# Kernel tuning notes

Hardware: AMD Instinct MI355X
Metric: run time of the kernel (lower is better)

Reference implementation:

```python
import jax, jax.numpy as jnp
from jax import lax
import numpy as np

T, B, IN, H = 192, 16, 256, 256


def setup_inputs() -> dict:
    key = jax.random.key(0)
    ks = jax.random.split(key, 8)
    s = 0.05  # small init scale to keep gates well-conditioned
    return {
        "x": jax.random.normal(ks[0], (T, B, IN), dtype=jnp.float32),
        # shared LSTM (PyTorch gate order i,f,g,o)
        "W_ih": jax.random.normal(ks[1], (4 * H, IN), dtype=jnp.float32) * s,
        "W_hh": jax.random.normal(ks[2], (4 * H, H), dtype=jnp.float32) * s,
        "b_lstm": jnp.zeros((4 * H,), dtype=jnp.float32),
        # additive attention: Ws: (IN+2H)->H, Us: H->1
        "Ws_w": jax.random.normal(ks[3], (H, IN + 2 * H), dtype=jnp.float32) * s,
        "Ws_b": jnp.zeros((H,), dtype=jnp.float32),
        "Us_w": jax.random.normal(ks[4], (1, H), dtype=jnp.float32) * s,
        "Us_b": jnp.zeros((1,), dtype=jnp.float32),
        # task-specific message LSTM cell: gates from concat(x_t, Rt, h_prev)
        "Wc": jax.random.normal(ks[5], (4 * H, IN + 2 * H), dtype=jnp.float32) * s,
        "bc": jnp.zeros((4 * H,), dtype=jnp.float32),
        "TASK": 0,
    }


def _lstm_gates(pre, c):
    i, f, g, o = jnp.split(pre, 4, axis=-1)
    i = jax.nn.sigmoid(i)
    f = jax.nn.sigmoid(f)
    g = jnp.tanh(g)
    o = jax.nn.sigmoid(o)
    c_new = f * c + i * g
    h_new = o * jnp.tanh(c_new)
    return h_new, c_new


def reference(x, W_ih, W_hh, b_lstm, Ws_w, Ws_b, Us_w, Us_b, Wc, bc, TASK):
    t_len, b, _ = x.shape
    h = W_hh.shape[1]

    h0 = jnp.zeros((b, h), x.dtype)

    # ---- shared LSTM over time ----
    def shared_step(carry, xt):
        hh, cc = carry
        pre = xt @ W_ih.T + hh @ W_hh.T + b_lstm
        hh, cc = _lstm_gates(pre, cc)
        return (hh, cc), hh

    (_, _), hs = lax.scan(shared_step, (h0, h0), x)  # hs: [T,B,H]

    # ---- per-timestep additive attention + message LSTM cell ----
    def task_step(carry, xt):
        hh, cc = carry
        h_task = jnp.broadcast_to(hh[None], (t_len, b, h))
        cat = jnp.concatenate([hs, h_task, x], axis=-1)          # [T,B,IN+2H]
        score = jnp.tanh(cat @ Ws_w.T + Ws_b) @ Us_w.T + Us_b    # [T,B,1]
        att = jax.nn.softmax(score, axis=0)                       # over time
        Rt = jnp.sum(att * hs, axis=0)                            # [B,H]
        pre = jnp.concatenate([xt, Rt, hh], axis=-1) @ Wc.T + bc
        hh, cc = _lstm_gates(pre, cc)
        return (hh, cc), hh

    (_, _), outs = lax.scan(task_step, (h0, h0), x)  # [T,B,H]
    return jnp.transpose(outs, (1, 0, 2))  # [B,T,H] (torch.stack axis=1)
```

## Files before the change

kernel.cpp:

```cpp
#include <hip/hip_runtime.h>
#include <hip/hip_fp16.h>

#define T_LEN 192

typedef unsigned long long u64;
typedef _Float16 f16x8 __attribute__((ext_vector_type(8)));
typedef float f32x4 __attribute__((ext_vector_type(4)));

#define OFF_X1F   0
#define OFF_XPRE  3145728
#define OFF_XB3   6291456
#define OFF_HSB   7077888
#define OFF_P     7864320
#define OFF_H     7921664
#define OFF_HX    7929856
#define OFF_HP    7946240
#define EXCH_WORDS 147456

#define SMEM_TASK 148736

__device__ __forceinline__ unsigned packh2(float a, float b){
  union { __half2 h; unsigned u; } v;
  v.h = __halves2half2(__float2half(a), __float2half(b));
  return v.u;
}
__device__ __forceinline__ float2 unp2(unsigned u){
  union { unsigned u32; __half2 h; } v; v.u32 = u;
  return __half22float2(v.h);
}
__device__ __forceinline__ float fdot2(unsigned a, unsigned b, float c){
#if __has_builtin(__builtin_amdgcn_fdot2)
  typedef _Float16 h2t __attribute__((ext_vector_type(2)));
  union { unsigned u; h2t h; } ua, ub;
  ua.u = a; ub.u = b;
  return __builtin_amdgcn_fdot2(ua.h, ub.h, c, false);
#else
  float2 x = unp2(a), y = unp2(b);
  return c + x.x*y.x + x.y*y.y;
#endif
}
__device__ __forceinline__ float tanh_f(float x){
  float cx = fminf(fmaxf(x, -15.f), 15.f);
  float e = __expf(2.f * cx);
  return (e - 1.f) / (e + 1.f);
}
__device__ __forceinline__ float sigm(float x){
  float cx = fminf(fmaxf(x, -30.f), 30.f);
  return 1.f / (1.f + __expf(-cx));
}

__device__ __forceinline__ u64 gld64(const u64* p){
  return __hip_atomic_load(p, __ATOMIC_RELAXED, __HIP_MEMORY_SCOPE_AGENT);
}
__device__ __forceinline__ void gst64(u64* p, u64 v){
  __hip_atomic_store(p, v, __ATOMIC_RELAXED, __HIP_MEMORY_SCOPE_AGENT);
}

__global__ __launch_bounds__(256) void initk(float* p, int n){
  int i = blockIdx.x * blockDim.x + threadIdx.x;
  int stride = gridDim.x * blockDim.x;
  for (; i < n; i += stride) p[i] = 0.f;
}

__global__ __launch_bounds__(256) void proj3m(const float* __restrict__ x,
                                              const float* __restrict__ W_ih,
                                              const float* __restrict__ b_l,
                                              const float* __restrict__ Wc,
                                              const float* __restrict__ bc,
                                              const float* __restrict__ Ws_w,
                                              const float* __restrict__ Ws_b,
                                              float* __restrict__ ws){
  __shared__ unsigned xhi[16 * 136];
  __shared__ unsigned xlo[16 * 136];
  const int bx = blockIdx.x, t = blockIdx.y, tid = threadIdx.x;

  {
    int row = tid >> 4, c0 = (tid & 15) * 16;
    const float* xp = &x[(t * 16 + row) * 256 + c0];
    #pragma unroll
    for (int i = 0; i < 8; ++i) {
      float2 v = *(const float2*)&xp[2 * i];
      _Float16 h0 = (_Float16)v.x, h1 = (_Float16)v.y;
      float l0 = v.x - (float)h0, l1 = v.y - (float)h1;
      union { _Float16 h[2]; unsigned u; } ph, pl;
      ph.h[0] = h0; ph.h[1] = h1;
      pl.h[0] = (_Float16)l0; pl.h[1] = (_Float16)l1;
      xhi[row * 136 + c0 / 2 + i] = ph.u;
      xlo[row * 136 + c0 / 2 + i] = pl.u;
    }
  }

  const int wave = tid >> 6, lane = tid & 63;
  const int b16 = lane & 15, quad = lane >> 4;
  const int n0 = bx * 64 + wave * 16;
  const float* wrow; const float* bias; int nb, mode;
  if (bx < 16)      { nb = n0;        wrow = &W_ih[(nb + b16) * 256];       bias = b_l;  mode = 0; }
  else if (bx < 32) { nb = n0 - 1024; wrow = &Wc[(nb + b16) * 768];         bias = bc;   mode = 1; }
  else              { nb = n0 - 2048; wrow = &Ws_w[(nb + b16) * 768 + 512]; bias = Ws_b; mode = 2; }

  f16x8 whi[8], wlo[8];
  #pragma unroll
  for (int kk = 0; kk < 8; ++kk) {
    const float* wp = wrow + kk * 32 + quad * 8;
    f16x8 h, l;
    #pragma unroll
    for (int j = 0; j < 8; ++j) {
      float v = wp[j];
      _Float16 hh = (_Float16)v;
      h[j] = hh; l[j] = (_Float16)(v - (float)hh);
    }
    whi[kk] = h; wlo[kk] = l;
  }
  f32x4 acc;
  #pragma unroll
  for (int r = 0; r < 4; ++r) acc[r] = bias[nb + quad * 4 + r];
  __syncthreads();

  #pragma unroll
  for (int kk = 0; kk < 8; ++kk) {
    union { uint4 u; f16x8 h; } bh, bl;
    bh.u = *(const uint4*)&xhi[b16 * 136 + kk * 16 + quad * 4];
    bl.u = *(const uint4*)&xlo[b16 * 136 + kk * 16 + quad * 4];
    acc = __builtin_amdgcn_mfma_f32_16x16x32_f16(whi[kk], bh.h, acc, 0, 0, 0);
    acc = __builtin_amdgcn_mfma_f32_16x16x32_f16(wlo[kk], bh.h, acc, 0, 0, 0);
    acc = __builtin_amdgcn_mfma_f32_16x16x32_f16(whi[kk], bl.h, acc, 0, 0, 0);
  }

  float4 res; res.x = acc[0]; res.y = acc[1]; res.z = acc[2]; res.w = acc[3];
  if (mode == 0) {
    *(float4*)&ws[OFF_X1F + (((u64)t * 64 + (n0 >> 4)) * 16 + b16) * 16 + quad * 4] = res;
  } else if (mode == 1) {
    *(float4*)&ws[OFF_XPRE + ((u64)t * 16 + b16) * 1024 + nb + quad * 4] = res;
  } else {
    *(float4*)&ws[OFF_XB3 + ((u64)t * 16 + b16) * 256 + nb + quad * 4] = res;
  }
}

__global__ __launch_bounds__(512) void lstm_kernel(const float* __restrict__ X1F,
                                                   const float* __restrict__ W_hh,
                                                   float* __restrict__ hsB,
                                                   u64* __restrict__ hx){
  __shared__ unsigned hT[16 * 136];
  const int tid = threadIdx.x;
  const int wg = blockIdx.x;
  const int wave = tid >> 6, lane = tid & 63;
  const int b16 = lane & 15, quad = lane >> 4;
  const int jb = wg * 8 + wave;
  const int peerbase = (1 - wg) * 64;

  f16x8 wf[4][8];
  #pragma unroll
  for (int g = 0; g < 4; ++g) {
    #pragma unroll
    for (int kk = 0; kk < 8; ++kk) {
      int row = g * 256 + jb * 16 + b16;
      const float* wp = &W_hh[row * 256 + kk * 32 + quad * 8];
      f16x8 v;
      #pragma unroll
      for (int j = 0; j < 8; ++j) v[j] = (_Float16)wp[j];
      wf[g][kk] = v;
    }
  }
  for (int i = tid; i < 16 * 136; i += 512) hT[i] = 0u;
  float cst[4] = {0.f, 0.f, 0.f, 0.f};
  __syncthreads();

  for (int t = 0; t < T_LEN; ++t) {
    float4 xi[4];
    #pragma unroll
    for (int g = 0; g < 4; ++g)
      xi[g] = *(const float4*)&X1F[((t * 64 + g * 16 + jb) * 16 + b16) * 16 + quad * 4];

    if (t > 0) {
      const u64* src = &hx[((u64)((t - 1) & 1)) * 2048];
      int bbq = tid >> 5, k2 = tid & 31;
      int jp0 = peerbase + 2 * k2;
      u64 v0, v1;
      for (;;) {
        v0 = gld64(&src[bbq * 128 + jp0]);
        v1 = gld64(&src[bbq * 128 + jp0 + 1]);
        if ((unsigned)v0 == (unsigned)t && (unsigned)v1 == (unsigned)t) break;
      }
      hT[bbq * 136 + jp0]     = (unsigned)(v0 >> 32);
      hT[bbq * 136 + jp0 + 1] = (unsigned)(v1 >> 32);
    }
    __syncthreads();

    f32x4 acc[4];
    #pragma unroll
    for (int g = 0; g < 4; ++g) {
      f32x4 a; a[0]=xi[g].x; a[1]=xi[g].y; a[2]=xi[g].z; a[3]=xi[g].w;
      acc[g] = a;
    }
    #pragma unroll
    for (int kk = 0; kk < 8; ++kk) {
      union { uint4 u; f16x8 h; } bv;
      bv.u = *(const uint4*)&hT[b16 * 136 + kk * 16 + quad * 4];
      #pragma unroll
      for (int g = 0; g < 4; ++g)
        acc[g] = __builtin_amdgcn_mfma_f32_16x16x32_f16(wf[g][kk], bv.h, acc[g], 0, 0, 0);
    }
    __syncthreads();

    float hv[4];
    #pragma unroll
    for (int r = 0; r < 4; ++r) {
      float pi = acc[0][r], pf = acc[1][r], pg = acc[2][r], po = acc[3][r];
      float cn = fmaf(sigm(pf), cst[r], sigm(pi) * tanh_f(pg));
      hv[r] = sigm(po) * tanh_f(cn);
      cst[r] = cn;
    }
    int j0 = jb * 16 + quad * 4;
    int jp = j0 >> 1;
    unsigned p01 = packh2(hv[0], hv[1]);
    unsigned p23 = packh2(hv[2], hv[3]);
    u64* dst = &hx[((u64)(t & 1)) * 2048];
    gst64(&dst[b16 * 128 + jp],     ((u64)p01 << 32) | (unsigned)(t + 1));
    gst64(&dst[b16 * 128 + jp + 1], ((u64)p23 << 32) | (unsigned)(t + 1));
    *(float4*)&hsB[(b16 * 192 + t) * 256 + j0] = make_float4(hv[0], hv[1], hv[2], hv[3]);
    hT[b16 * 136 + jp]     = p01;
    hT[b16 * 136 + jp + 1] = p23;
  }
}

__global__ __launch_bounds__(1024) void task_kernel(
    const float* __restrict__ xb3, const float* __restrict__ xpre,
    const float* __restrict__ hsB, const float* __restrict__ Us_w,
    const float* __restrict__ Us_b, const float* __restrict__ Wc,
    const float* __restrict__ Ws_w,
    u64* __restrict__ Pbuf, u64* __restrict__ Hbuf, u64* __restrict__ HPbuf,
    float* __restrict__ out){
  extern __shared__ char smem[];
  unsigned* hsL  = (unsigned*)smem;
  unsigned* Ws1L = (unsigned*)(smem + 99072);
  float*    baseS= (float*)(smem + 115584);
  unsigned* WcH  = (unsigned*)smem;
  unsigned* Ws2P = (unsigned*)(smem + 65536);
  float* prel    = (float*)(smem + 82944);
  float* eel     = (float*)(smem + 89600);
  unsigned* h2l  = (unsigned*)(smem + 90368);
  unsigned* h2own= (unsigned*)(smem + 90880);
  float* hterml  = (float*)(smem + 90944);
  float* usl     = (float*)(smem + 91072);
  float* msc     = (float*)(smem + 91200);
  unsigned* G2   = (unsigned*)(smem + 99072);

  const int tid = threadIdx.x;
  const int bb = blockIdx.x & 15;
  const int s  = blockIdx.x >> 4;

  for (int idx = tid; idx < 24576; idx += 1024) {
    int tp = idx >> 7, k2 = idx & 127;
    const float* hp = &hsB[(bb * 192 + tp) * 256 + 2 * k2];
    hsL[tp * 129 + k2] = packh2(hp[0], hp[1]);
  }
  for (int idx = tid; idx < 4096; idx += 1024) {
    int c = idx >> 7, k2 = idx & 127;
    const float* wp = &Ws_w[(32 * s + c) * 768 + 2 * k2];
    Ws1L[c * 129 + k2] = packh2(wp[0], wp[1]);
  }
  __syncthreads();
  {
    int c = tid & 31, g = tid >> 5;
    float a6[6];
    #pragma unroll
    for (int j = 0; j < 6; ++j)
      a6[j] = xb3[((g * 6 + j) * 16 + bb) * 256 + 32 * s + c];
    for (int k2 = 0; k2 < 128; ++k2) {
      unsigned wv = Ws1L[c * 129 + k2];
      #pragma unroll
      for (int j = 0; j < 6; ++j)
        a6[j] = fdot2(wv, hsL[(g * 6 + j) * 129 + k2], a6[j]);
    }
    #pragma unroll
    for (int j = 0; j < 6; ++j)
      baseS[(g * 6 + j) * 33 + c] = a6[j];
  }
  __syncthreads();
  unsigned bs4[4] = {0u, 0u, 0u, 0u};
  if (tid < 768) {
    int tp = tid >> 2, q = tid & 3;
    #pragma unroll
    for (int j2 = 0; j2 < 4; ++j2)
      bs4[j2] = packh2(baseS[tp * 33 + q * 8 + 2 * j2],
                       baseS[tp * 33 + q * 8 + 2 * j2 + 1]);
  }
  __syncthreads();
  {
    int l = tid & 127, tg = tid >> 7;
    int row = (l >> 5) * 256 + 32 * s + (l & 31);
    const float* wr = &Wc[row * 768 + 256];
    float acc[24];
    #pragma unroll
    for (int i = 0; i < 24; ++i) acc[i] = 0.f;
    for (int kc = 0; kc < 128; kc += 16) {
      unsigned wv[16];
      #pragma unroll
      for (int i = 0; i < 16; ++i) {
        float2 wp2 = *(const float2*)&wr[2 * (kc + i)];
        wv[i] = packh2(wp2.x, wp2.y);
      }
      #pragma unroll
      for (int tt = 0; tt < 24; ++tt) {
        const unsigned* hp = &hsL[(tg * 24 + tt) * 129 + kc];
        float a = acc[tt];
        #pragma unroll
        for (int i = 0; i < 16; ++i) a = fdot2(wv[i], hp[i], a);
        acc[tt] = a;
      }
    }
    #pragma unroll
    for (int i = 0; i < 12; ++i)
      G2[l * 97 + tg * 12 + i] = packh2(acc[2 * i], acc[2 * i + 1]);
  }
  __syncthreads();
  for (int idx = tid; idx < 16384; idx += 1024) {
    int j = idx & 3, l = (idx >> 2) & 127, k2q = idx >> 9;
    int k2 = k2q * 4 + j;
    int row = (l >> 5) * 256 + 32 * s + (l & 31);
    const float* wp = &Wc[row * 768 + 512 + 2 * k2];
    WcH[idx] = packh2(wp[0], wp[1]);
  }
  for (int idx = tid; idx < 4096; idx += 1024) {
    int c = idx >> 4, j = idx & 15;
    const float* wp = &Ws_w[c * 768 + 256 + 2 * (16 * s + j)];
    Ws2P[c * 17 + j] = packh2(wp[0], wp[1]);
  }
  if (tid < 32) usl[tid] = Us_w[32 * s + tid];
  const float usb = Us_b[0];
  __syncthreads();

  u64* Pb  = Pbuf + (bb * 8) * 192;
  u64* Hb  = Hbuf + bb * 256;
  u64* HPb = HPbuf + (bb * 8) * 256;
  const uint4* wp4 = (const uint4*)WcH;
  const uint4* av4 = (const uint4*)h2l;
  float creg = 0.f;

  for (int t = 0; t < T_LEN; ++t) {
    const unsigned seq = (unsigned)(t + 1);
    float xp0 = 0.f, xp1 = 0.f, xp2 = 0.f, xp3 = 0.f;
    if (tid < 32) {
      const float* xq = &xpre[(t * 16 + bb) * 1024 + 32 * s + tid];
      xp0 = xq[0]; xp1 = xq[256]; xp2 = xq[512]; xp3 = xq[768];
    }
    if (t > 0) {
      if (tid < 256) {
        int c = tid >> 3, sp = tid & 7;
        u64 v;
        do { v = gld64(&HPb[sp * 256 + 32 * s + c]); } while ((unsigned)v != (unsigned)t);
        float a = __uint_as_float((unsigned)(v >> 32));
        a += __shfl_xor(a, 1); a += __shfl_xor(a, 2); a += __shfl_xor(a, 4);
        if (sp == 0) hterml[c] = a;
      } else if (tid < 512) {
        int col = tid - 256;
        u64 v;
        do { v = gld64(&Hb[col]); } while ((unsigned)v != (unsigned)t);
        float hvv = __uint_as_float((unsigned)(v >> 32));
        float hp_ = __shfl_xor(hvv, 1);
        if ((col & 1) == 0) h2l[col >> 1] = packh2(hvv, hp_);
      }
    } else {
      if (tid < 32) hterml[tid] = 0.f;
      if (tid < 128) h2l[tid] = 0u;
    }
    __syncthreads();
    if (tid < 768) {
      int tp = tid >> 2, q = tid & 3;
      float p = 0.f;
      #pragma unroll
      for (int m = 0; m < 4; ++m) {
        float2 bv = unp2(bs4[m]);
        int c0 = q * 8 + 2 * m;
        p += usl[c0]     * tanh_f(bv.x + hterml[c0]);
        p += usl[c0 + 1] * tanh_f(bv.y + hterml[c0 + 1]);
      }
      p += __shfl_xor(p, 1);
      p += __shfl_xor(p, 2);
      if ((tid & 3) == 0)
        gst64(&Pb[s * 192 + tp], ((u64)__float_as_uint(p) << 32) | seq);
    }
    {
      int l = tid & 127, kq = tid >> 7;
      float a = 0.f;
      #pragma unroll
      for (int i = 0; i < 4; ++i) {
        uint4 w4 = wp4[(kq * 4 + i) * 128 + l];
        uint4 a4 = av4[kq * 4 + i];
        a = fdot2(w4.x, a4.x, a); a = fdot2(w4.y, a4.y, a);
        a = fdot2(w4.z, a4.z, a); a = fdot2(w4.w, a4.w, a);
      }
      prel[l * 13 + kq] = a;
    }
    if (tid < 192) {
      u64 v[8];
      for (;;) {
        bool ok = true;
        #pragma unroll
        for (int sp = 0; sp < 8; ++sp) {
          v[sp] = gld64(&Pb[sp * 192 + tid]);
          ok &= ((unsigned)v[sp] == seq);
        }
        if (ok) break;
      }
      float sum = 0.f;
      #pragma unroll
      for (int sp = 0; sp < 8; ++sp) sum += __uint_as_float((unsigned)(v[sp] >> 32));
      eel[tid] = __expf(sum + usb);
    }
    __syncthreads();
    if (tid < 64) {
      float aa = eel[tid] + eel[tid + 64] + eel[tid + 128];
      #pragma unroll
      for (int off = 32; off >= 1; off >>= 1) aa += __shfl_xor(aa, off);
      if (tid == 0) msc[0] = 1.f / aa;
    }
    if (tid >= 512) {
      int l = (tid - 512) & 127, tq = (tid - 512) >> 7;
      const unsigned* gp = &G2[l * 97 + tq * 24];
      const float2* ep = (const float2*)&eel[tq * 48];
      float a = 0.f;
      #pragma unroll
      for (int i = 0; i < 24; ++i) {
        float2 g = unp2(gp[i]);
        float2 e = ep[i];
        a = fmaf(g.x, e.x, a); a = fmaf(g.y, e.y, a);
      }
      prel[l * 13 + 8 + tq] = a;
    }
    __syncthreads();
    if (tid < 32) {
      float m = msc[0];
      float pr[4];
      #pragma unroll
      for (int g = 0; g < 4; ++g) {
        const float* pp = &prel[(g * 32 + tid) * 13];
        float hsum = pp[0] + pp[1] + pp[2] + pp[3] + pp[4] + pp[5] + pp[6] + pp[7];
        float gsum = pp[8] + pp[9] + pp[10] + pp[11];
        pr[g] = hsum + m * gsum;
      }
      pr[0] += xp0; pr[1] += xp1; pr[2] += xp2; pr[3] += xp3;
      float cn = fmaf(sigm(pr[1]), creg, sigm(pr[0]) * tanh_f(pr[2]));
      float hh = sigm(pr[3]) * tanh_f(cn);
      creg = cn;
      gst64(&Hb[32 * s + tid], ((u64)__float_as_uint(hh) << 32) | seq);
      out[(bb * 192 + t) * 256 + 32 * s + tid] = hh;
      float hp_ = __shfl_xor(hh, 1);
      if ((tid & 1) == 0) h2own[tid >> 1] = packh2(hh, hp_);
    }
    __syncthreads();
    if (tid < 256) {
      float a = 0.f;
      const unsigned* wp = &Ws2P[tid * 17];
      #pragma unroll
      for (int j = 0; j < 16; ++j) a = fdot2(wp[j], h2own[j], a);
      gst64(&HPb[s * 256 + tid], ((u64)__float_as_uint(a) << 32) | seq);
    }
  }
}

extern "C" void kernel_launch(void* const* d_in, const int* in_sizes, int n_in,
                              void* d_out, int out_size, void* d_ws, size_t ws_size,
                              hipStream_t stream) {
  (void)in_sizes; (void)n_in; (void)out_size; (void)ws_size;
  const float* x    = (const float*)d_in[0];
  const float* W_ih = (const float*)d_in[1];
  const float* W_hh = (const float*)d_in[2];
  const float* b_l  = (const float*)d_in[3];
  const float* Ws_w = (const float*)d_in[4];
  const float* Ws_b = (const float*)d_in[5];
  const float* Us_w = (const float*)d_in[6];
  const float* Us_b = (const float*)d_in[7];
  const float* Wc   = (const float*)d_in[8];
  const float* bc   = (const float*)d_in[9];
  float* out = (float*)d_out;
  float* ws = (float*)d_ws;

  hipFuncSetAttribute((const void*)task_kernel,
                      hipFuncAttributeMaxDynamicSharedMemorySize, 160 * 1024);

  initk<<<64, 256, 0, stream>>>(ws + OFF_P, EXCH_WORDS);

  proj3m<<<dim3(36, 192), 256, 0, stream>>>(x, W_ih, b_l, Wc, bc, Ws_w, Ws_b, ws);

  lstm_kernel<<<2, 512, 0, stream>>>(ws + OFF_X1F, W_hh, ws + OFF_HSB,
                                     (u64*)(ws + OFF_HX));

  task_kernel<<<128, 1024, SMEM_TASK, stream>>>(
      ws + OFF_XB3, ws + OFF_XPRE, ws + OFF_HSB, Us_w, Us_b, Wc, Ws_w,
      (u64*)(ws + OFF_P), (u64*)(ws + OFF_H), (u64*)(ws + OFF_HP), out);
}
```

Before: 1.653 ms.

## Drop cross-block score exchange, overlap own-half LSTM MFMA with peer wait, batch projection timesteps

The task kernel now has each block compute the full 256-column attention score for its timesteps locally. It keeps all 32 packed base-score pairs in registers and reads all hterm columns, which removes the per-step global score exchange and its spin-wait across 8 peer blocks. The shared LSTM kernel issues the MFMAs for its own half of h before polling the peer block's half, so the wait overlaps compute. The projection kernel handles two timesteps per block to reuse the converted weights. The costs are more registers in the task kernel, a longer one-time base-score precompute that loops over all 8 slices, and an extra barrier per LSTM step.

```diff
diff --git a/kernel.cpp b/kernel.cpp
--- a/kernel.cpp
+++ b/kernel.cpp
@@ -70,13 +70,14 @@
                                               const float* __restrict__ Ws_w,
                                               const float* __restrict__ Ws_b,
                                               float* __restrict__ ws){
-  __shared__ unsigned xhi[16 * 136];
-  __shared__ unsigned xlo[16 * 136];
-  const int bx = blockIdx.x, t = blockIdx.y, tid = threadIdx.x;
-
-  {
+  __shared__ unsigned xhi[2][16 * 136];
+  __shared__ unsigned xlo[2][16 * 136];
+  const int bx = blockIdx.x, t0 = blockIdx.y * 2, tid = threadIdx.x;
+
+  #pragma unroll
+  for (int tt = 0; tt < 2; ++tt) {
     int row = tid >> 4, c0 = (tid & 15) * 16;
-    const float* xp = &x[(t * 16 + row) * 256 + c0];
+    const float* xp = &x[((t0 + tt) * 16 + row) * 256 + c0];
     #pragma unroll
     for (int i = 0; i < 8; ++i) {
       float2 v = *(const float2*)&xp[2 * i];
@@ -85,8 +86,8 @@
       union { _Float16 h[2]; unsigned u; } ph, pl;
       ph.h[0] = h0; ph.h[1] = h1;
       pl.h[0] = (_Float16)l0; pl.h[1] = (_Float16)l1;
-      xhi[row * 136 + c0 / 2 + i] = ph.u;
-      xlo[row * 136 + c0 / 2 + i] = pl.u;
+      xhi[tt][row * 136 + c0 / 2 + i] = ph.u;
+      xlo[tt][row * 136 + c0 / 2 + i] = pl.u;
     }
   }
 
@@ -111,28 +112,37 @@
     }
     whi[kk] = h; wlo[kk] = l;
   }
-  f32x4 acc;
-  #pragma unroll
-  for (int r = 0; r < 4; ++r) acc[r] = bias[nb + quad * 4 + r];
+  f32x4 acc[2];
+  #pragma unroll
+  for (int tt = 0; tt < 2; ++tt)
+    #pragma unroll
+    for (int r = 0; r < 4; ++r) acc[tt][r] = bias[nb + quad * 4 + r];
   __syncthreads();
 
   #pragma unroll
   for (int kk = 0; kk < 8; ++kk) {
-    union { uint4 u; f16x8 h; } bh, bl;
-    bh.u = *(const uint4*)&xhi[b16 * 136 + kk * 16 + quad * 4];
-    bl.u = *(const uint4*)&xlo[b16 * 136 + kk * 16 + quad * 4];
-    acc = __builtin_amdgcn_mfma_f32_16x16x32_f16(whi[kk], bh.h, acc, 0, 0, 0);
-    acc = __builtin_amdgcn_mfma_f32_16x16x32_f16(wlo[kk], bh.h, acc, 0, 0, 0);
-    acc = __builtin_amdgcn_mfma_f32_16x16x32_f16(whi[kk], bl.h, acc, 0, 0, 0);
-  }
-
-  float4 res; res.x = acc[0]; res.y = acc[1]; res.z = acc[2]; res.w = acc[3];
-  if (mode == 0) {
-    *(float4*)&ws[OFF_X1F + (((u64)t * 64 + (n0 >> 4)) * 16 + b16) * 16 + quad * 4] = res;
-  } else if (mode == 1) {
-    *(float4*)&ws[OFF_XPRE + ((u64)t * 16 + b16) * 1024 + nb + quad * 4] = res;
-  } else {
-    *(float4*)&ws[OFF_XB3 + ((u64)t * 16 + b16) * 256 + nb + quad * 4] = res;
+    #pragma unroll
+    for (int tt = 0; tt < 2; ++tt) {
+      union { uint4 u; f16x8 h; } bh, bl;
+      bh.u = *(const uint4*)&xhi[tt][b16 * 136 + kk * 16 + quad * 4];
+      bl.u = *(const uint4*)&xlo[tt][b16 * 136 + kk * 16 + quad * 4];
+      acc[tt] = __builtin_amdgcn_mfma_f32_16x16x32_f16(whi[kk], bh.h, acc[tt], 0, 0, 0);
+      acc[tt] = __builtin_amdgcn_mfma_f32_16x16x32_f16(wlo[kk], bh.h, acc[tt], 0, 0, 0);
+      acc[tt] = __builtin_amdgcn_mfma_f32_16x16x32_f16(whi[kk], bl.h, acc[tt], 0, 0, 0);
+    }
+  }
+
+  #pragma unroll
+  for (int tt = 0; tt < 2; ++tt) {
+    int t = t0 + tt;
+    float4 res; res.x = acc[tt][0]; res.y = acc[tt][1]; res.z = acc[tt][2]; res.w = acc[tt][3];
+    if (mode == 0) {
+      *(float4*)&ws[OFF_X1F + (((u64)t * 64 + (n0 >> 4)) * 16 + b16) * 16 + quad * 4] = res;
+    } else if (mode == 1) {
+      *(float4*)&ws[OFF_XPRE + ((u64)t * 16 + b16) * 1024 + nb + quad * 4] = res;
+    } else {
+      *(float4*)&ws[OFF_XB3 + ((u64)t * 16 + b16) * 256 + nb + quad * 4] = res;
+    }
   }
 }
 
@@ -147,6 +157,7 @@
   const int b16 = lane & 15, quad = lane >> 4;
   const int jb = wg * 8 + wave;
   const int peerbase = (1 - wg) * 64;
+  const int ownk0 = wg * 4, peerk0 = (1 - wg) * 4;
 
   f16x8 wf[4][8];
   #pragma unroll
@@ -170,6 +181,20 @@
     #pragma unroll
     for (int g = 0; g < 4; ++g)
       xi[g] = *(const float4*)&X1F[((t * 64 + g * 16 + jb) * 16 + b16) * 16 + quad * 4];
+
+    f32x4 acc[4];
+    #pragma unroll
+    for (int g = 0; g < 4; ++g) { f32x4 z = {0.f, 0.f, 0.f, 0.f}; acc[g] = z; }
+
+    #pragma unroll
+    for (int kk2 = 0; kk2 < 4; ++kk2) {
+      int kk = ownk0 + kk2;
+      union { uint4 u; f16x8 h; } bv;
+      bv.u = *(const uint4*)&hT[b16 * 136 + kk * 16 + quad * 4];
+      #pragma unroll
+      for (int g = 0; g < 4; ++g)
+        acc[g] = __builtin_amdgcn_mfma_f32_16x16x32_f16(wf[g][kk], bv.h, acc[g], 0, 0, 0);
+    }
 
     if (t > 0) {
       const u64* src = &hx[((u64)((t - 1) & 1)) * 2048];
@@ -186,26 +211,23 @@
     }
     __syncthreads();
 
-    f32x4 acc[4];
-    #pragma unroll
-    for (int g = 0; g < 4; ++g) {
-      f32x4 a; a[0]=xi[g].x; a[1]=xi[g].y; a[2]=xi[g].z; a[3]=xi[g].w;
-      acc[g] = a;
-    }
-    #pragma unroll
-    for (int kk = 0; kk < 8; ++kk) {
+    #pragma unroll
+    for (int kk2 = 0; kk2 < 4; ++kk2) {
+      int kk = peerk0 + kk2;
       union { uint4 u; f16x8 h; } bv;
       bv.u = *(const uint4*)&hT[b16 * 136 + kk * 16 + quad * 4];
       #pragma unroll
       for (int g = 0; g < 4; ++g)
         acc[g] = __builtin_amdgcn_mfma_f32_16x16x32_f16(wf[g][kk], bv.h, acc[g], 0, 0, 0);
     }
-    __syncthreads();
 
     float hv[4];
     #pragma unroll
     for (int r = 0; r < 4; ++r) {
-      float pi = acc[0][r], pf = acc[1][r], pg = acc[2][r], po = acc[3][r];
+      float pi = acc[0][r] + ((const float*)&xi[0])[r];
+      float pf = acc[1][r] + ((const float*)&xi[1])[r];
+      float pg = acc[2][r] + ((const float*)&xi[2])[r];
+      float po = acc[3][r] + ((const float*)&xi[3])[r];
       float cn = fmaf(sigm(pf), cst[r], sigm(pi) * tanh_f(pg));
       hv[r] = sigm(po) * tanh_f(cn);
       cst[r] = cn;
@@ -220,6 +242,7 @@
     *(float4*)&hsB[(b16 * 192 + t) * 256 + j0] = make_float4(hv[0], hv[1], hv[2], hv[3]);
     hT[b16 * 136 + jp]     = p01;
     hT[b16 * 136 + jp + 1] = p23;
+    __syncthreads();
   }
 }
 
@@ -228,7 +251,7 @@
     const float* __restrict__ hsB, const float* __restrict__ Us_w,
     const float* __restrict__ Us_b, const float* __restrict__ Wc,
     const float* __restrict__ Ws_w,
-    u64* __restrict__ Pbuf, u64* __restrict__ Hbuf, u64* __restrict__ HPbuf,
+    u64* __restrict__ Hbuf, u64* __restrict__ HPbuf,
     float* __restrict__ out){
   extern __shared__ char smem[];
   unsigned* hsL  = (unsigned*)smem;
@@ -237,12 +260,12 @@
   unsigned* WcH  = (unsigned*)smem;
   unsigned* Ws2P = (unsigned*)(smem + 65536);
   float* prel    = (float*)(smem + 82944);
-  float* eel     = (float*)(smem + 89600);
-  unsigned* h2l  = (unsigned*)(smem + 90368);
-  unsigned* h2own= (unsigned*)(smem + 90880);
-  float* hterml  = (float*)(smem + 90944);
-  float* usl     = (float*)(smem + 91072);
-  float* msc     = (float*)(smem + 91200);
+  float* eel     = (float*)(smem + 86528);
+  unsigned* h2l  = (unsigned*)(smem + 87296);
+  unsigned* h2own= (unsigned*)(smem + 87808);
+  float* hterml  = (float*)(smem + 87872);
+  float* usl     = (float*)(smem + 88896);
+  float* msc     = (float*)(smem + 89920);
   unsigned* G2   = (unsigned*)(smem + 99072);
 
   const int tid = threadIdx.x;
@@ -254,38 +277,44 @@
     const float* hp = &hsB[(bb * 192 + tp) * 256 + 2 * k2];
     hsL[tp * 129 + k2] = packh2(hp[0], hp[1]);
   }
-  for (int idx = tid; idx < 4096; idx += 1024) {
-    int c = idx >> 7, k2 = idx & 127;
-    const float* wp = &Ws_w[(32 * s + c) * 768 + 2 * k2];
-    Ws1L[c * 129 + k2] = packh2(wp[0], wp[1]);
-  }
   __syncthreads();
-  {
-    int c = tid & 31, g = tid >> 5;
-    float a6[6];
-    #pragma unroll
-    for (int j = 0; j < 6; ++j)
-      a6[j] = xb3[((g * 6 + j) * 16 + bb) * 256 + 32 * s + c];
-    for (int k2 = 0; k2 < 128; ++k2) {
-      unsigned wv = Ws1L[c * 129 + k2];
+  unsigned bs[32];
+  #pragma unroll
+  for (int i = 0; i < 32; ++i) bs[i] = 0u;
+  #pragma unroll
+  for (int p = 0; p < 8; ++p) {
+    for (int idx = tid; idx < 4096; idx += 1024) {
+      int c = idx >> 7, k2 = idx & 127;
+      const float* wp = &Ws_w[(32 * p + c) * 768 + 2 * k2];
+      Ws1L[c * 129 + k2] = packh2(wp[0], wp[1]);
+    }
+    __syncthreads();
+    {
+      int c = tid & 31, g = tid >> 5;
+      float a6[6];
       #pragma unroll
       for (int j = 0; j < 6; ++j)
-        a6[j] = fdot2(wv, hsL[(g * 6 + j) * 129 + k2], a6[j]);
-    }
-    #pragma unroll
-    for (int j = 0; j < 6; ++j)
-      baseS[(g * 6 + j) * 33 + c] = a6[j];
-  }
-  __syncthreads();
-  unsigned bs4[4] = {0u, 0u, 0u, 0u};
-  if (tid < 768) {
-    int tp = tid >> 2, q = tid & 3;
-    #pragma unroll
-    for (int j2 = 0; j2 < 4; ++j2)
-      bs4[j2] = packh2(baseS[tp * 33 + q * 8 + 2 * j2],
-                       baseS[tp * 33 + q * 8 + 2 * j2 + 1]);
-  }
-  __syncthreads();
+        a6[j] = xb3[((g * 6 + j) * 16 + bb) * 256 + 32 * p + c];
+      for (int k2 = 0; k2 < 128; ++k2) {
+        unsigned wv = Ws1L[c * 129 + k2];
+        #pragma unroll
+        for (int j = 0; j < 6; ++j)
+          a6[j] = fdot2(wv, hsL[(g * 6 + j) * 129 + k2], a6[j]);
+      }
+      #pragma unroll
+      for (int j = 0; j < 6; ++j)
+        baseS[(g * 6 + j) * 33 + c] = a6[j];
+    }
+    __syncthreads();
+    if (tid < 768 && (tid & 3) == (p >> 1)) {
+      int tp = tid >> 2;
+      #pragma unroll
+      for (int i = 0; i < 16; ++i)
+        bs[(p & 1) * 16 + i] =
+            packh2(baseS[tp * 33 + 2 * i], baseS[tp * 33 + 2 * i + 1]);
+    }
+    __syncthreads();
+  }
   {
     int l = tid & 127, tg = tid >> 7;
     int row = (l >> 5) * 256 + 32 * s + (l & 31);
@@ -326,11 +355,10 @@
     const float* wp = &Ws_w[c * 768 + 256 + 2 * (16 * s + j)];
     Ws2P[c * 17 + j] = packh2(wp[0], wp[1]);
   }
-  if (tid < 32) usl[tid] = Us_w[32 * s + tid];
+  if (tid < 256) usl[tid] = Us_w[tid];
   const float usb = Us_b[0];
   __syncthreads();
 
-  u64* Pb  = Pbuf + (bb * 8) * 192;
   u64* Hb  = Hbuf + bb * 256;
   u64* HPb = HPbuf + (bb * 8) * 256;
   const uint4* wp4 = (const uint4*)WcH;
@@ -345,15 +373,25 @@
       xp0 = xq[0]; xp1 = xq[256]; xp2 = xq[512]; xp3 = xq[768];
     }
     if (t > 0) {
-      if (tid < 256) {
-        int c = tid >> 3, sp = tid & 7;
-        u64 v;
-        do { v = gld64(&HPb[sp * 256 + 32 * s + c]); } while ((unsigned)v != (unsigned)t);
-        float a = __uint_as_float((unsigned)(v >> 32));
-        a += __shfl_xor(a, 1); a += __shfl_xor(a, 2); a += __shfl_xor(a, 4);
-        if (sp == 0) hterml[c] = a;
-      } else if (tid < 512) {
-        int col = tid - 256;
+      if (tid < 512) {
+        int c = tid >> 1, sp0 = (tid & 1) * 4;
+        u64 v0, v1, v2, v3;
+        for (;;) {
+          v0 = gld64(&HPb[(sp0 + 0) * 256 + c]);
+          v1 = gld64(&HPb[(sp0 + 1) * 256 + c]);
+          v2 = gld64(&HPb[(sp0 + 2) * 256 + c]);
+          v3 = gld64(&HPb[(sp0 + 3) * 256 + c]);
+          if ((unsigned)v0 == (unsigned)t && (unsigned)v1 == (unsigned)t &&
+              (unsigned)v2 == (unsigned)t && (unsigned)v3 == (unsigned)t) break;
+        }
+        float a = __uint_as_float((unsigned)(v0 >> 32)) +
+                  __uint_as_float((unsigned)(v1 >> 32)) +
+                  __uint_as_float((unsigned)(v2 >> 32)) +
+                  __uint_as_float((unsigned)(v3 >> 32));
+        a += __shfl_xor(a, 1);
+        if ((tid & 1) == 0) hterml[c] = a;
+      } else if (tid < 768) {
+        int col = tid - 512;
         u64 v;
         do { v = gld64(&Hb[col]); } while ((unsigned)v != (unsigned)t);
         float hvv = __uint_as_float((unsigned)(v >> 32));
@@ -361,52 +399,36 @@
         if ((col & 1) == 0) h2l[col >> 1] = packh2(hvv, hp_);
       }
     } else {
-      if (tid < 32) hterml[tid] = 0.f;
+      if (tid < 256) hterml[tid] = 0.f;
       if (tid < 128) h2l[tid] = 0u;
     }
     __syncthreads();
     if (tid < 768) {
       int tp = tid >> 2, q = tid & 3;
+      int c0b = q * 64;
       float p = 0.f;
       #pragma unroll
-      for (int m = 0; m < 4; ++m) {
-        float2 bv = unp2(bs4[m]);
-        int c0 = q * 8 + 2 * m;
+      for (int i = 0; i < 32; ++i) {
+        float2 bv = unp2(bs[i]);
+        int c0 = c0b + 2 * i;
         p += usl[c0]     * tanh_f(bv.x + hterml[c0]);
         p += usl[c0 + 1] * tanh_f(bv.y + hterml[c0 + 1]);
       }
       p += __shfl_xor(p, 1);
       p += __shfl_xor(p, 2);
-      if ((tid & 3) == 0)
-        gst64(&Pb[s * 192 + tp], ((u64)__float_as_uint(p) << 32) | seq);
-    }
-    {
-      int l = tid & 127, kq = tid >> 7;
+      if (q == 0) eel[tp] = __expf(p + usb);
+    } else {
+      int r = tid - 768;
+      int l = r & 127, kq = r >> 7;
       float a = 0.f;
       #pragma unroll
-      for (int i = 0; i < 4; ++i) {
-        uint4 w4 = wp4[(kq * 4 + i) * 128 + l];
-        uint4 a4 = av4[kq * 4 + i];
+      for (int i = 0; i < 16; ++i) {
+        uint4 w4 = wp4[(kq * 16 + i) * 128 + l];
+        uint4 a4 = av4[kq * 16 + i];
         a = fdot2(w4.x, a4.x, a); a = fdot2(w4.y, a4.y, a);
         a = fdot2(w4.z, a4.z, a); a = fdot2(w4.w, a4.w, a);
       }
-      prel[l * 13 + kq] = a;
-    }
-    if (tid < 192) {
-      u64 v[8];
-      for (;;) {
-        bool ok = true;
-        #pragma unroll
-        for (int sp = 0; sp < 8; ++sp) {
-          v[sp] = gld64(&Pb[sp * 192 + tid]);
-          ok &= ((unsigned)v[sp] == seq);
-        }
-        if (ok) break;
-      }
-      float sum = 0.f;
-      #pragma unroll
-      for (int sp = 0; sp < 8; ++sp) sum += __uint_as_float((unsigned)(v[sp] >> 32));
-      eel[tid] = __expf(sum + usb);
+      prel[l * 7 + kq] = a;
     }
     __syncthreads();
     if (tid < 64) {
@@ -426,7 +448,7 @@
         float2 e = ep[i];
         a = fmaf(g.x, e.x, a); a = fmaf(g.y, e.y, a);
       }
-      prel[l * 13 + 8 + tq] = a;
+      prel[l * 7 + 2 + tq] = a;
     }
     __syncthreads();
     if (tid < 32) {
@@ -434,9 +456,9 @@
       float pr[4];
       #pragma unroll
       for (int g = 0; g < 4; ++g) {
-        const float* pp = &prel[(g * 32 + tid) * 13];
-        float hsum = pp[0] + pp[1] + pp[2] + pp[3] + pp[4] + pp[5] + pp[6] + pp[7];
-        float gsum = pp[8] + pp[9] + pp[10] + pp[11];
+        const float* pp = &prel[(g * 32 + tid) * 7];
+        float hsum = pp[0] + pp[1];
+        float gsum = pp[2] + pp[3] + pp[4] + pp[5];
         pr[g] = hsum + m * gsum;
       }
       pr[0] += xp0; pr[1] += xp1; pr[2] += xp2; pr[3] += xp3;
@@ -481,12 +503,12 @@
 
   initk<<<64, 256, 0, stream>>>(ws + OFF_P, EXCH_WORDS);
 
-  proj3m<<<dim3(36, 192), 256, 0, stream>>>(x, W_ih, b_l, Wc, bc, Ws_w, Ws_b, ws);
+  proj3m<<<dim3(36, 96), 256, 0, stream>>>(x, W_ih, b_l, Wc, bc, Ws_w, Ws_b, ws);
 
   lstm_kernel<<<2, 512, 0, stream>>>(ws + OFF_X1F, W_hh, ws + OFF_HSB,
                                      (u64*)(ws + OFF_HX));
 
   task_kernel<<<128, 1024, SMEM_TASK, stream>>>(
       ws + OFF_XB3, ws + OFF_XPRE, ws + OFF_HSB, Us_w, Us_b, Wc, Ws_w,
-      (u64*)(ws + OFF_P), (u64*)(ws + OFF_H), (u64*)(ws + OFF_HP), out);
-}
+      (u64*)(ws + OFF_H), (u64*)(ws + OFF_HP), out);
+}
```

New measurement: 5.681 ms. 244% more time.

## Process two timesteps per projection block and add sleep backoff in spin-waits

Applied to the files above, without the earlier changes.

The input projection kernel now handles two timesteps per workgroup, so the split weight registers are loaded and converted once per pair of timesteps and the grid is halved. Separately, every cross-workgroup spin-wait in the LSTM and task kernels now issues s_sleep between polls, which cuts memory-system pressure from busy polling. The sleep can add wake-up latency on the serial critical path of the recurrent loops.

```diff
diff --git a/kernel.cpp b/kernel.cpp
--- a/kernel.cpp
+++ b/kernel.cpp
@@ -70,13 +70,14 @@
                                               const float* __restrict__ Ws_w,
                                               const float* __restrict__ Ws_b,
                                               float* __restrict__ ws){
-  __shared__ unsigned xhi[16 * 136];
-  __shared__ unsigned xlo[16 * 136];
-  const int bx = blockIdx.x, t = blockIdx.y, tid = threadIdx.x;
-
-  {
+  __shared__ unsigned xhi[2][16 * 136];
+  __shared__ unsigned xlo[2][16 * 136];
+  const int bx = blockIdx.x, t0 = blockIdx.y * 2, tid = threadIdx.x;
+
+  #pragma unroll
+  for (int tt = 0; tt < 2; ++tt) {
     int row = tid >> 4, c0 = (tid & 15) * 16;
-    const float* xp = &x[(t * 16 + row) * 256 + c0];
+    const float* xp = &x[((t0 + tt) * 16 + row) * 256 + c0];
     #pragma unroll
     for (int i = 0; i < 8; ++i) {
       float2 v = *(const float2*)&xp[2 * i];
@@ -85,8 +86,8 @@
       union { _Float16 h[2]; unsigned u; } ph, pl;
       ph.h[0] = h0; ph.h[1] = h1;
       pl.h[0] = (_Float16)l0; pl.h[1] = (_Float16)l1;
-      xhi[row * 136 + c0 / 2 + i] = ph.u;
-      xlo[row * 136 + c0 / 2 + i] = pl.u;
+      xhi[tt][row * 136 + c0 / 2 + i] = ph.u;
+      xlo[tt][row * 136 + c0 / 2 + i] = pl.u;
     }
   }
 
@@ -111,28 +112,37 @@
     }
     whi[kk] = h; wlo[kk] = l;
   }
-  f32x4 acc;
+  f32x4 acc[2];
   #pragma unroll
-  for (int r = 0; r < 4; ++r) acc[r] = bias[nb + quad * 4 + r];
+  for (int tt = 0; tt < 2; ++tt)
+    #pragma unroll
+    for (int r = 0; r < 4; ++r) acc[tt][r] = bias[nb + quad * 4 + r];
   __syncthreads();
 
   #pragma unroll
   for (int kk = 0; kk < 8; ++kk) {
-    union { uint4 u; f16x8 h; } bh, bl;
-    bh.u = *(const uint4*)&xhi[b16 * 136 + kk * 16 + quad * 4];
-    bl.u = *(const uint4*)&xlo[b16 * 136 + kk * 16 + quad * 4];
-    acc = __builtin_amdgcn_mfma_f32_16x16x32_f16(whi[kk], bh.h, acc, 0, 0, 0);
-    acc = __builtin_amdgcn_mfma_f32_16x16x32_f16(wlo[kk], bh.h, acc, 0, 0, 0);
-    acc = __builtin_amdgcn_mfma_f32_16x16x32_f16(whi[kk], bl.h, acc, 0, 0, 0);
-  }
-
-  float4 res; res.x = acc[0]; res.y = acc[1]; res.z = acc[2]; res.w = acc[3];
-  if (mode == 0) {
-    *(float4*)&ws[OFF_X1F + (((u64)t * 64 + (n0 >> 4)) * 16 + b16) * 16 + quad * 4] = res;
-  } else if (mode == 1) {
-    *(float4*)&ws[OFF_XPRE + ((u64)t * 16 + b16) * 1024 + nb + quad * 4] = res;
-  } else {
-    *(float4*)&ws[OFF_XB3 + ((u64)t * 16 + b16) * 256 + nb + quad * 4] = res;
+    #pragma unroll
+    for (int tt = 0; tt < 2; ++tt) {
+      union { uint4 u; f16x8 h; } bh, bl;
+      bh.u = *(const uint4*)&xhi[tt][b16 * 136 + kk * 16 + quad * 4];
+      bl.u = *(const uint4*)&xlo[tt][b16 * 136 + kk * 16 + quad * 4];
+      acc[tt] = __builtin_amdgcn_mfma_f32_16x16x32_f16(whi[kk], bh.h, acc[tt], 0, 0, 0);
+      acc[tt] = __builtin_amdgcn_mfma_f32_16x16x32_f16(wlo[kk], bh.h, acc[tt], 0, 0, 0);
+      acc[tt] = __builtin_amdgcn_mfma_f32_16x16x32_f16(whi[kk], bl.h, acc[tt], 0, 0, 0);
+    }
+  }
+
+  #pragma unroll
+  for (int tt = 0; tt < 2; ++tt) {
+    int t = t0 + tt;
+    float4 res; res.x = acc[tt][0]; res.y = acc[tt][1]; res.z = acc[tt][2]; res.w = acc[tt][3];
+    if (mode == 0) {
+      *(float4*)&ws[OFF_X1F + (((u64)t * 64 + (n0 >> 4)) * 16 + b16) * 16 + quad * 4] = res;
+    } else if (mode == 1) {
+      *(float4*)&ws[OFF_XPRE + ((u64)t * 16 + b16) * 1024 + nb + quad * 4] = res;
+    } else {
+      *(float4*)&ws[OFF_XB3 + ((u64)t * 16 + b16) * 256 + nb + quad * 4] = res;
+    }
   }
 }
 
@@ -175,11 +185,12 @@
       const u64* src = &hx[((u64)((t - 1) & 1)) * 2048];
       int bbq = tid >> 5, k2 = tid & 31;
       int jp0 = peerbase + 2 * k2;
-      u64 v0, v1;
-      for (;;) {
+      u64 v0 = gld64(&src[bbq * 128 + jp0]);
+      u64 v1 = gld64(&src[bbq * 128 + jp0 + 1]);
+      while ((unsigned)v0 != (unsigned)t || (unsigned)v1 != (unsigned)t) {
+        __builtin_amdgcn_s_sleep(1);
         v0 = gld64(&src[bbq * 128 + jp0]);
         v1 = gld64(&src[bbq * 128 + jp0 + 1]);
-        if ((unsigned)v0 == (unsigned)t && (unsigned)v1 == (unsigned)t) break;
       }
       hT[bbq * 136 + jp0]     = (unsigned)(v0 >> 32);
       hT[bbq * 136 + jp0 + 1] = (unsigned)(v1 >> 32);
@@ -347,15 +358,21 @@
     if (t > 0) {
       if (tid < 256) {
         int c = tid >> 3, sp = tid & 7;
-        u64 v;
-        do { v = gld64(&HPb[sp * 256 + 32 * s + c]); } while ((unsigned)v != (unsigned)t);
+        u64 v = gld64(&HPb[sp * 256 + 32 * s + c]);
+        while ((unsigned)v != (unsigned)t) {
+          __builtin_amdgcn_s_sleep(1);
+          v = gld64(&HPb[sp * 256 + 32 * s + c]);
+        }
         float a = __uint_as_float((unsigned)(v >> 32));
         a += __shfl_xor(a, 1); a += __shfl_xor(a, 2); a += __shfl_xor(a, 4);
         if (sp == 0) hterml[c] = a;
       } else if (tid < 512) {
         int col = tid - 256;
-        u64 v;
-        do { v = gld64(&Hb[col]); } while ((unsigned)v != (unsigned)t);
+        u64 v = gld64(&Hb[col]);
+        while ((unsigned)v != (unsigned)t) {
+          __builtin_amdgcn_s_sleep(1);
+          v = gld64(&Hb[col]);
+        }
         float hvv = __uint_as_float((unsigned)(v >> 32));
         float hp_ = __shfl_xor(hvv, 1);
         if ((col & 1) == 0) h2l[col >> 1] = packh2(hvv, hp_);
@@ -402,6 +419,7 @@
           ok &= ((unsigned)v[sp] == seq);
         }
         if (ok) break;
+        __builtin_amdgcn_s_sleep(1);
       }
       float sum = 0.f;
       #pragma unroll
@@ -481,7 +499,7 @@
 
   initk<<<64, 256, 0, stream>>>(ws + OFF_P, EXCH_WORDS);
 
-  proj3m<<<dim3(36, 192), 256, 0, stream>>>(x, W_ih, b_l, Wc, bc, Ws_w, Ws_b, ws);
+  proj3m<<<dim3(36, 96), 256, 0, stream>>>(x, W_ih, b_l, Wc, bc, Ws_w, Ws_b, ws);
 
   lstm_kernel<<<2, 512, 0, stream>>>(ws + OFF_X1F, W_hh, ws + OFF_HSB,
                                      (u64*)(ws + OFF_HX));
```

New measurement: 1.630 ms. About the same (-1.4%).
